# Performance work log

Measured on AMD Instinct MI355X. Metric: run time of the kernel, lower is better.

## Reference

```python
import jax, jax.numpy as jnp
import numpy as np

KERNEL_SIZE = 5
GROUP_SIZE = 1
SCALE = 2


def setup_inputs() -> dict:
    key = jax.random.key(0)
    k1, k2 = jax.random.split(key)
    features = jax.random.normal(k1, (8, 256, 64, 64), dtype=jnp.float32)
    masks = jax.random.uniform(k2, (8, KERNEL_SIZE * KERNEL_SIZE * GROUP_SIZE, 64 * SCALE, 64 * SCALE), dtype=jnp.float32)
    return {"features": features, "masks": masks}


def _carafe_naive(features, masks, k, g, s):
    n, c, h, w = features.shape
    cg = c // g
    pad = (k - 1) // 2
    fp = jnp.pad(features, ((0, 0), (0, 0), (pad, pad), (pad, pad)))
    # im2col patches, matching F.unfold ordering: channel outer, kernel
    # positions row-major inner -> [n, c, k*k, h, w]
    patches = jnp.stack(
        [fp[:, :, i:i + h, j:j + w] for i in range(k) for j in range(k)],
        axis=2,
    )
    feat = patches.reshape(n, g, cg, k * k, h, w)          # n g c i h w
    ker = masks.reshape(n, g, k * k, h, s, w, s)           # n g i h a w b
    # per-pixel dynamic conv over the k*k window, fused with upsample
    out = jnp.einsum('ngcihw,ngihawb->ngchawb', feat, ker)  # n g c h a w b
    return out.reshape(n, c, h * s, w * s)


def reference(features, masks):
    return _carafe_naive(features, masks, KERNEL_SIZE, GROUP_SIZE, SCALE)
```

## Files before the change

### kernel.cpp

```cpp
#include <hip/hip_runtime.h>

#define K 5
#define N_ 8
#define C_ 256
#define H_ 64
#define W_ 64
#define HW (H_ * W_)
#define HO 128
#define WO 128
#define HOWO (HO * WO)
#define HB 8
#define WB 32
#define CCHUNK 32
#define UC 8
#define NGROUP (CCHUNK / UC)
#define LDS_R (HB + K - 1)
#define LDS_C (WB + K - 1)
#define POS (LDS_R * LDS_C)

typedef __attribute__((ext_vector_type(2))) float f2;

__global__ __launch_bounds__(256)
void carafe_quad_kernel(const float* __restrict__ feat,
                        const float* __restrict__ mask,
                        float* __restrict__ out) {
    const int wt = blockIdx.x;
    const int ht = blockIdx.y;
    const int zc = blockIdx.z;
    const int n  = zc >> 3;
    const int c0 = (zc & 7) * CCHUNK;
    const int h0 = ht * HB;
    const int w0 = wt * WB;

    const int tid = threadIdx.x;
    const int r   = tid >> 5;
    const int c   = tid & 31;
    const int hb  = h0 + r;
    const int wb  = w0 + c;

    f2 m0[K * K], m1[K * K];
    {
        const f2* mb = (const f2*)(mask + (size_t)n * (K * K) * HOWO
                                        + (size_t)(2 * hb) * WO + 2 * wb);
        #pragma unroll
        for (int i = 0; i < K * K; ++i) {
            m0[i] = mb[(size_t)i * (HOWO / 2)];
            m1[i] = mb[(size_t)i * (HOWO / 2) + WO / 2];
        }
    }

    int off0, off1;
    bool v0, v1, has1;
    {
        int p  = tid;
        int rr = p / LDS_C, cc = p - rr * LDS_C;
        int hs = h0 - 2 + rr, ws = w0 - 2 + cc;
        v0   = (hs >= 0 && hs < H_ && ws >= 0 && ws < W_);
        off0 = hs * W_ + ws;
    }
    has1 = (tid + 256) < POS;
    {
        int p  = tid + 256;
        int rr = p / LDS_C, cc = p - rr * LDS_C;
        int hs = h0 - 2 + rr, ws = w0 - 2 + cc;
        v1   = has1 && (hs >= 0 && hs < H_ && ws >= 0 && ws < W_);
        off1 = hs * W_ + ws;
    }

    __shared__ float4 lds[2][2][POS];

    const float* fbase = feat + (size_t)n * C_ * HW;
    float*       obase = out  + (size_t)n * C_ * HOWO
                              + (size_t)(2 * hb) * WO + 2 * wb;

    float s0[UC], s1[UC];
    auto stage_load = [&](int cbase) {
        const float* fp = fbase + (size_t)cbase * HW;
        #pragma unroll
        for (int u = 0; u < UC; ++u) s0[u] = v0 ? fp[u * HW + off0] : 0.f;
        #pragma unroll
        for (int u = 0; u < UC; ++u) s1[u] = v1 ? fp[u * HW + off1] : 0.f;
    };
    auto stage_write = [&](int buf) {
        lds[buf][0][tid] = make_float4(s0[0], s0[1], s0[2], s0[3]);
        lds[buf][1][tid] = make_float4(s0[4], s0[5], s0[6], s0[7]);
        if (has1) {
            lds[buf][0][tid + 256] = make_float4(s1[0], s1[1], s1[2], s1[3]);
            lds[buf][1][tid + 256] = make_float4(s1[4], s1[5], s1[6], s1[7]);
        }
    };

    stage_load(c0);
    stage_write(0);
    __syncthreads();

    const int rbase = r * LDS_C + c;

    for (int g = 0; g < NGROUP; ++g) {
        const int buf = g & 1;

        if (g + 1 < NGROUP) stage_load(c0 + (g + 1) * UC);

        #pragma unroll
        for (int s = 0; s < 2; ++s) {
            const float4* Ls = &lds[buf][s][rbase];
            f2 a0[4], a1[4];
            #pragma unroll
            for (int u = 0; u < 4; ++u) { a0[u] = (f2)0.f; a1[u] = (f2)0.f; }
            #pragma unroll
            for (int ki = 0; ki < K; ++ki) {
                #pragma unroll
                for (int kj = 0; kj < K; ++kj) {
                    float4 f  = Ls[ki * LDS_C + kj];
                    f2 w0m = m0[ki * K + kj];
                    f2 w1m = m1[ki * K + kj];
                    a0[0] += f.x * w0m;  a1[0] += f.x * w1m;
                    a0[1] += f.y * w0m;  a1[1] += f.y * w1m;
                    a0[2] += f.z * w0m;  a1[2] += f.z * w1m;
                    a0[3] += f.w * w0m;  a1[3] += f.w * w1m;
                }
            }
            #pragma unroll
            for (int u = 0; u < 4; ++u) {
                f2* op = (f2*)(obase + (size_t)(c0 + g * UC + s * 4 + u) * HOWO);
                __builtin_nontemporal_store(a0[u], op);
                __builtin_nontemporal_store(a1[u], op + WO / 2);
            }
        }

        if (g + 1 < NGROUP) {
            stage_write(buf ^ 1);
            __syncthreads();
        }
    }
}

extern "C" void kernel_launch(void* const* d_in, const int* in_sizes, int n_in,
                              void* d_out, int out_size, void* d_ws, size_t ws_size,
                              hipStream_t stream) {
    const float* feat = (const float*)d_in[0];
    const float* mask = (const float*)d_in[1];
    float* out = (float*)d_out;

    dim3 grid(W_ / WB, H_ / HB, N_ * (C_ / CCHUNK));
    dim3 block(256);
    carafe_quad_kernel<<<grid, block, 0, stream>>>(feat, mask, out);
}
```

Before: 45.90 us.

## Flatten channel loop into grid with one 8-channel group per block

```diff
diff --git a/kernel.cpp b/kernel.cpp
--- a/kernel.cpp
+++ b/kernel.cpp
@@ -11,9 +11,7 @@
 #define HOWO (HO * WO)
 #define HB 8
 #define WB 32
-#define CCHUNK 32
 #define UC 8
-#define NGROUP (CCHUNK / UC)
 #define LDS_R (HB + K - 1)
 #define LDS_C (WB + K - 1)
 #define POS (LDS_R * LDS_C)
@@ -21,14 +19,14 @@
 typedef __attribute__((ext_vector_type(2))) float f2;
 
 __global__ __launch_bounds__(256)
-void carafe_quad_kernel(const float* __restrict__ feat,
+void carafe_flat_kernel(const float* __restrict__ feat,
                         const float* __restrict__ mask,
                         float* __restrict__ out) {
     const int wt = blockIdx.x;
     const int ht = blockIdx.y;
     const int zc = blockIdx.z;
-    const int n  = zc >> 3;
-    const int c0 = (zc & 7) * CCHUNK;
+    const int n  = zc >> 5;
+    const int c0 = (zc & 31) * UC;
     const int h0 = ht * HB;
     const int w0 = wt * WB;
 
@@ -37,17 +35,6 @@
     const int c   = tid & 31;
     const int hb  = h0 + r;
     const int wb  = w0 + c;
-
-    f2 m0[K * K], m1[K * K];
-    {
-        const f2* mb = (const f2*)(mask + (size_t)n * (K * K) * HOWO
-                                        + (size_t)(2 * hb) * WO + 2 * wb);
-        #pragma unroll
-        for (int i = 0; i < K * K; ++i) {
-            m0[i] = mb[(size_t)i * (HOWO / 2)];
-            m1[i] = mb[(size_t)i * (HOWO / 2) + WO / 2];
-        }
-    }
 
     int off0, off1;
     bool v0, v1, has1;
@@ -67,71 +54,60 @@
         off1 = hs * W_ + ws;
     }
 
-    __shared__ float4 lds[2][2][POS];
+    __shared__ float4 lds[2][POS];
 
-    const float* fbase = feat + (size_t)n * C_ * HW;
-    float*       obase = out  + (size_t)n * C_ * HOWO
-                              + (size_t)(2 * hb) * WO + 2 * wb;
+    const float* fbase = feat + (size_t)n * C_ * HW + (size_t)c0 * HW;
 
-    float s0[UC], s1[UC];
-    auto stage_load = [&](int cbase) {
-        const float* fp = fbase + (size_t)cbase * HW;
+    {
+        float s0[UC], s1[UC];
         #pragma unroll
-        for (int u = 0; u < UC; ++u) s0[u] = v0 ? fp[u * HW + off0] : 0.f;
+        for (int u = 0; u < UC; ++u) s0[u] = v0 ? fbase[u * HW + off0] : 0.f;
         #pragma unroll
-        for (int u = 0; u < UC; ++u) s1[u] = v1 ? fp[u * HW + off1] : 0.f;
-    };
-    auto stage_write = [&](int buf) {
-        lds[buf][0][tid] = make_float4(s0[0], s0[1], s0[2], s0[3]);
-        lds[buf][1][tid] = make_float4(s0[4], s0[5], s0[6], s0[7]);
+        for (int u = 0; u < UC; ++u) s1[u] = v1 ? fbase[u * HW + off1] : 0.f;
+        lds[0][tid] = make_float4(s0[0], s0[1], s0[2], s0[3]);
+        lds[1][tid] = make_float4(s0[4], s0[5], s0[6], s0[7]);
         if (has1) {
-            lds[buf][0][tid + 256] = make_float4(s1[0], s1[1], s1[2], s1[3]);
-            lds[buf][1][tid + 256] = make_float4(s1[4], s1[5], s1[6], s1[7]);
+            lds[0][tid + 256] = make_float4(s1[0], s1[1], s1[2], s1[3]);
+            lds[1][tid + 256] = make_float4(s1[4], s1[5], s1[6], s1[7]);
         }
-    };
-
-    stage_load(c0);
-    stage_write(0);
+    }
     __syncthreads();
 
+    const f2* mb = (const f2*)(mask + (size_t)n * (K * K) * HOWO
+                                    + (size_t)(2 * hb) * WO + 2 * wb);
     const int rbase = r * LDS_C + c;
 
-    for (int g = 0; g < NGROUP; ++g) {
-        const int buf = g & 1;
+    f2 a0[UC], a1[UC];
+    #pragma unroll
+    for (int u = 0; u < UC; ++u) { a0[u] = (f2)0.f; a1[u] = (f2)0.f; }
 
-        if (g + 1 < NGROUP) stage_load(c0 + (g + 1) * UC);
+    #pragma unroll
+    for (int ki = 0; ki < K; ++ki) {
+        #pragma unroll
+        for (int kj = 0; kj < K; ++kj) {
+            const int i = ki * K + kj;
+            f2 m0 = mb[(size_t)i * (HOWO / 2)];
+            f2 m1 = mb[(size_t)i * (HOWO / 2) + WO / 2];
+            float4 fA = lds[0][rbase + ki * LDS_C + kj];
+            float4 fB = lds[1][rbase + ki * LDS_C + kj];
+            a0[0] += fA.x * m0;  a1[0] += fA.x * m1;
+            a0[1] += fA.y * m0;  a1[1] += fA.y * m1;
+            a0[2] += fA.z * m0;  a1[2] += fA.z * m1;
+            a0[3] += fA.w * m0;  a1[3] += fA.w * m1;
+            a0[4] += fB.x * m0;  a1[4] += fB.x * m1;
+            a0[5] += fB.y * m0;  a1[5] += fB.y * m1;
+            a0[6] += fB.z * m0;  a1[6] += fB.z * m1;
+            a0[7] += fB.w * m0;  a1[7] += fB.w * m1;
+        }
+    }
 
-        #pragma unroll
-        for (int s = 0; s < 2; ++s) {
-            const float4* Ls = &lds[buf][s][rbase];
-            f2 a0[4], a1[4];
-            #pragma unroll
-            for (int u = 0; u < 4; ++u) { a0[u] = (f2)0.f; a1[u] = (f2)0.f; }
-            #pragma unroll
-            for (int ki = 0; ki < K; ++ki) {
-                #pragma unroll
-                for (int kj = 0; kj < K; ++kj) {
-                    float4 f  = Ls[ki * LDS_C + kj];
-                    f2 w0m = m0[ki * K + kj];
-                    f2 w1m = m1[ki * K + kj];
-                    a0[0] += f.x * w0m;  a1[0] += f.x * w1m;
-                    a0[1] += f.y * w0m;  a1[1] += f.y * w1m;
-                    a0[2] += f.z * w0m;  a1[2] += f.z * w1m;
-                    a0[3] += f.w * w0m;  a1[3] += f.w * w1m;
-                }
-            }
-            #pragma unroll
-            for (int u = 0; u < 4; ++u) {
-                f2* op = (f2*)(obase + (size_t)(c0 + g * UC + s * 4 + u) * HOWO);
-                __builtin_nontemporal_store(a0[u], op);
-                __builtin_nontemporal_store(a1[u], op + WO / 2);
-            }
-        }
-
-        if (g + 1 < NGROUP) {
-            stage_write(buf ^ 1);
-            __syncthreads();
-        }
+    float* obase = out + (size_t)n * C_ * HOWO + (size_t)c0 * HOWO
+                       + (size_t)(2 * hb) * WO + 2 * wb;
+    #pragma unroll
+    for (int u = 0; u < UC; ++u) {
+        f2* op = (f2*)(obase + (size_t)u * HOWO);
+        __builtin_nontemporal_store(a0[u], op);
+        __builtin_nontemporal_store(a1[u], op + WO / 2);
     }
 }
 
@@ -142,7 +118,7 @@
     const float* mask = (const float*)d_in[1];
     float* out = (float*)d_out;
 
-    dim3 grid(W_ / WB, H_ / HB, N_ * (C_ / CCHUNK));
+    dim3 grid(W_ / WB, H_ / HB, N_ * (C_ / UC));
     dim3 block(256);
-    carafe_quad_kernel<<<grid, block, 0, stream>>>(feat, mask, out);
+    carafe_flat_kernel<<<grid, block, 0, stream>>>(feat, mask, out);
 }
```

Measured after the change: 51.93 us. +13.1%, slower.

## Give each wavefront a private LDS halo tile to eliminate block barriers

Applied to the files above, without the earlier changes.

```diff
diff --git a/kernel.cpp b/kernel.cpp
--- a/kernel.cpp
+++ b/kernel.cpp
@@ -12,16 +12,16 @@
 #define HB 8
 #define WB 32
 #define CCHUNK 32
-#define UC 8
-#define NGROUP (CCHUNK / UC)
-#define LDS_R (HB + K - 1)
+#define UC 4
+#define NG (CCHUNK / UC)
+#define HALO_R 6
 #define LDS_C (WB + K - 1)
-#define POS (LDS_R * LDS_C)
+#define WPOS (HALO_R * LDS_C)
 
 typedef __attribute__((ext_vector_type(2))) float f2;
 
 __global__ __launch_bounds__(256)
-void carafe_quad_kernel(const float* __restrict__ feat,
+void carafe_wave_kernel(const float* __restrict__ feat,
                         const float* __restrict__ mask,
                         float* __restrict__ out) {
     const int wt = blockIdx.x;
@@ -32,105 +32,94 @@
     const int h0 = ht * HB;
     const int w0 = wt * WB;
 
-    const int tid = threadIdx.x;
-    const int r   = tid >> 5;
-    const int c   = tid & 31;
-    const int hb  = h0 + r;
-    const int wb  = w0 + c;
+    const int tid  = threadIdx.x;
+    const int wave = tid >> 6;
+    const int lane = tid & 63;
+    const int r    = tid >> 5;
+    const int c    = tid & 31;
+    const int hb   = h0 + r;
+    const int wb   = w0 + c;
 
     f2 m0[K * K], m1[K * K];
-    {
-        const f2* mb = (const f2*)(mask + (size_t)n * (K * K) * HOWO
-                                        + (size_t)(2 * hb) * WO + 2 * wb);
-        #pragma unroll
-        for (int i = 0; i < K * K; ++i) {
-            m0[i] = mb[(size_t)i * (HOWO / 2)];
-            m1[i] = mb[(size_t)i * (HOWO / 2) + WO / 2];
-        }
+    const f2* mb = (const f2*)(mask + (size_t)n * (K * K) * HOWO
+                                    + (size_t)(2 * hb) * WO + 2 * wb);
+    #pragma unroll
+    for (int i = 0; i < K * K; ++i) {
+        m0[i] = mb[(size_t)i * (HOWO / 2)];
+        m1[i] = mb[(size_t)i * (HOWO / 2) + WO / 2];
     }
 
-    int off0, off1;
-    bool v0, v1, has1;
-    {
-        int p  = tid;
+    int  off[4];
+    bool val[4];
+    #pragma unroll
+    for (int i = 0; i < 4; ++i) {
+        int p  = i * 64 + lane;
         int rr = p / LDS_C, cc = p - rr * LDS_C;
-        int hs = h0 - 2 + rr, ws = w0 - 2 + cc;
-        v0   = (hs >= 0 && hs < H_ && ws >= 0 && ws < W_);
-        off0 = hs * W_ + ws;
-    }
-    has1 = (tid + 256) < POS;
-    {
-        int p  = tid + 256;
-        int rr = p / LDS_C, cc = p - rr * LDS_C;
-        int hs = h0 - 2 + rr, ws = w0 - 2 + cc;
-        v1   = has1 && (hs >= 0 && hs < H_ && ws >= 0 && ws < W_);
-        off1 = hs * W_ + ws;
+        int hs = h0 + 2 * wave - 2 + rr;
+        int ws = w0 - 2 + cc;
+        val[i] = (p < WPOS) && (hs >= 0) && (hs < H_) && (ws >= 0) && (ws < W_);
+        off[i] = hs * W_ + ws;
     }
 
-    __shared__ float4 lds[2][2][POS];
+    __shared__ float4 lds[4][2][WPOS];
 
     const float* fbase = feat + (size_t)n * C_ * HW;
-    float*       obase = out  + (size_t)n * C_ * HOWO
-                              + (size_t)(2 * hb) * WO + 2 * wb;
 
-    float s0[UC], s1[UC];
-    auto stage_load = [&](int cbase) {
-        const float* fp = fbase + (size_t)cbase * HW;
+    float s[4][UC];
+    auto load_group = [&](int cb) {
+        const float* fp = fbase + (size_t)cb * HW;
         #pragma unroll
-        for (int u = 0; u < UC; ++u) s0[u] = v0 ? fp[u * HW + off0] : 0.f;
+        for (int i = 0; i < 4; ++i)
+            #pragma unroll
+            for (int u = 0; u < UC; ++u)
+                s[i][u] = val[i] ? fp[u * HW + off[i]] : 0.f;
+    };
+    auto write_group = [&](int buf) {
         #pragma unroll
-        for (int u = 0; u < UC; ++u) s1[u] = v1 ? fp[u * HW + off1] : 0.f;
-    };
-    auto stage_write = [&](int buf) {
-        lds[buf][0][tid] = make_float4(s0[0], s0[1], s0[2], s0[3]);
-        lds[buf][1][tid] = make_float4(s0[4], s0[5], s0[6], s0[7]);
-        if (has1) {
-            lds[buf][0][tid + 256] = make_float4(s1[0], s1[1], s1[2], s1[3]);
-            lds[buf][1][tid + 256] = make_float4(s1[4], s1[5], s1[6], s1[7]);
+        for (int i = 0; i < 4; ++i) {
+            int p = i * 64 + lane;
+            if (p < WPOS)
+                lds[wave][buf][p] = make_float4(s[i][0], s[i][1], s[i][2], s[i][3]);
         }
     };
 
-    stage_load(c0);
-    stage_write(0);
-    __syncthreads();
+    load_group(c0);
+    write_group(0);
 
-    const int rbase = r * LDS_C + c;
+    float* obase = out + (size_t)n * C_ * HOWO + (size_t)(2 * hb) * WO + 2 * wb;
+    const int rbase = (r & 1) * LDS_C + c;
 
-    for (int g = 0; g < NGROUP; ++g) {
+    for (int g = 0; g < NG; ++g) {
         const int buf = g & 1;
 
-        if (g + 1 < NGROUP) stage_load(c0 + (g + 1) * UC);
+        if (g + 1 < NG) load_group(c0 + (g + 1) * UC);
 
+        const float4* Ls = &lds[wave][buf][rbase];
+        f2 a0[UC], a1[UC];
         #pragma unroll
-        for (int s = 0; s < 2; ++s) {
-            const float4* Ls = &lds[buf][s][rbase];
-            f2 a0[4], a1[4];
+        for (int u = 0; u < UC; ++u) { a0[u] = (f2)0.f; a1[u] = (f2)0.f; }
+        #pragma unroll
+        for (int ki = 0; ki < K; ++ki) {
             #pragma unroll
-            for (int u = 0; u < 4; ++u) { a0[u] = (f2)0.f; a1[u] = (f2)0.f; }
-            #pragma unroll
-            for (int ki = 0; ki < K; ++ki) {
-                #pragma unroll
-                for (int kj = 0; kj < K; ++kj) {
-                    float4 f  = Ls[ki * LDS_C + kj];
-                    f2 w0m = m0[ki * K + kj];
-                    f2 w1m = m1[ki * K + kj];
-                    a0[0] += f.x * w0m;  a1[0] += f.x * w1m;
-                    a0[1] += f.y * w0m;  a1[1] += f.y * w1m;
-                    a0[2] += f.z * w0m;  a1[2] += f.z * w1m;
-                    a0[3] += f.w * w0m;  a1[3] += f.w * w1m;
-                }
-            }
-            #pragma unroll
-            for (int u = 0; u < 4; ++u) {
-                f2* op = (f2*)(obase + (size_t)(c0 + g * UC + s * 4 + u) * HOWO);
-                __builtin_nontemporal_store(a0[u], op);
-                __builtin_nontemporal_store(a1[u], op + WO / 2);
+            for (int kj = 0; kj < K; ++kj) {
+                float4 f  = Ls[ki * LDS_C + kj];
+                f2 w0m = m0[ki * K + kj];
+                f2 w1m = m1[ki * K + kj];
+                a0[0] += f.x * w0m;  a1[0] += f.x * w1m;
+                a0[1] += f.y * w0m;  a1[1] += f.y * w1m;
+                a0[2] += f.z * w0m;  a1[2] += f.z * w1m;
+                a0[3] += f.w * w0m;  a1[3] += f.w * w1m;
             }
         }
 
-        if (g + 1 < NGROUP) {
-            stage_write(buf ^ 1);
-            __syncthreads();
+        if (g + 1 < NG) write_group(buf ^ 1);
+
+        float* oc = obase + (size_t)(c0 + g * UC) * HOWO;
+        #pragma unroll
+        for (int u = 0; u < UC; ++u) {
+            f2* op = (f2*)(oc + (size_t)u * HOWO);
+            __builtin_nontemporal_store(a0[u], op);
+            __builtin_nontemporal_store(a1[u], op + WO / 2);
         }
     }
 }
@@ -144,5 +133,5 @@
 
     dim3 grid(W_ / WB, H_ / HB, N_ * (C_ / CCHUNK));
     dim3 block(256);
-    carafe_quad_kernel<<<grid, block, 0, stream>>>(feat, mask, out);
+    carafe_wave_kernel<<<grid, block, 0, stream>>>(feat, mask, out);
 }
```

Result: slower. 47.00 us (+2.4%).
